# Kernel tuning notes

Measured on AMD Instinct MI355X. Metric: run time of the kernel, lower is better.

Reference implementation:

```python
import jax, jax.numpy as jnp
import numpy as np

IN_FEATURES = 4096
OUT_FEATURES = 16384
BATCH, SEQ = 2, 2048


def make_24_mask(w):
    # 2:4 structured mask: keep the 2 largest-magnitude entries of each
    # contiguous group of 4 along the in_features axis (like bdense2sparse).
    o, i = w.shape
    g = jnp.abs(w).reshape(o, i // 4, 4)
    # rank within each group; keep top-2
    idx = jnp.argsort(g, axis=-1)  # ascending
    ranks = jnp.argsort(idx, axis=-1)
    mask = ranks >= 2
    return mask.reshape(o, i)


def setup_inputs() -> dict:
    key = jax.random.key(0)
    k1, k2, k3 = jax.random.split(key, 3)
    x = jax.random.normal(k1, (BATCH, SEQ, IN_FEATURES), dtype=jnp.float32)
    weight = jax.random.normal(k2, (OUT_FEATURES, IN_FEATURES), dtype=jnp.float32) * (1.0 / np.sqrt(IN_FEATURES))
    mask = make_24_mask(weight)
    bias = jax.random.normal(k3, (OUT_FEATURES,), dtype=jnp.float32) * 0.01
    return {"x": x, "weight": weight, "mask": mask, "bias": bias}


def reference(x, weight, mask, bias):
    # 2:4 structured-sparse linear: y = x @ (mask * W).T + b
    w = weight * mask.astype(weight.dtype)
    out = jnp.einsum('bsi,oi->bso', x, w)  # [B, S, out_features]
    return out + bias
```

## Files before the change

kernel.cpp:

```cpp
#include <hip/hip_runtime.h>
#include <stdint.h>

#define M_DIM 4096
#define N_DIM 16384
#define K_DIM 4096

#define BM 128
#define BN 128
#define BK 64

typedef __attribute__((ext_vector_type(8))) short bf16x8;
typedef __attribute__((ext_vector_type(4))) float f32x4;


static __device__ __forceinline__ unsigned short f2bf(float f) {
    unsigned int u = __float_as_uint(f);
    return (unsigned short)((u + 0x7FFFu + ((u >> 16) & 1u)) >> 16);
}

typedef __attribute__((address_space(3))) void lds_void_t;
typedef const __attribute__((address_space(1))) void gbl_void_t;

static __device__ __forceinline__ void gload_lds16(const void* g, void* s) {
    __builtin_amdgcn_global_load_lds((gbl_void_t*)g, (lds_void_t*)s, 16, 0, 0);
}


__global__ void cvt_x_kernel(const float* __restrict__ x,
                             unsigned short* __restrict__ xb, int n8) {
    int i = blockIdx.x * blockDim.x + threadIdx.x;
    if (i >= n8) return;
    const float4 v0 = ((const float4*)x)[2 * i + 0];
    const float4 v1 = ((const float4*)x)[2 * i + 1];
    uint4 pk;
    pk.x = (unsigned)f2bf(v0.x) | ((unsigned)f2bf(v0.y) << 16);
    pk.y = (unsigned)f2bf(v0.z) | ((unsigned)f2bf(v0.w) << 16);
    pk.z = (unsigned)f2bf(v1.x) | ((unsigned)f2bf(v1.y) << 16);
    pk.w = (unsigned)f2bf(v1.z) | ((unsigned)f2bf(v1.w) << 16);
    ((uint4*)xb)[i] = pk;
}

__global__ void cvt_w_kernel(const float* __restrict__ w,
                             unsigned short* __restrict__ wb, int ngroups) {
    int g = blockIdx.x * blockDim.x + threadIdx.x;
    if (g >= ngroups) return;
    const float4 v = ((const float4*)w)[g];
    float a0 = fabsf(v.x), a1 = fabsf(v.y), a2 = fabsf(v.z), a3 = fabsf(v.w);
    int r0 = (a1 < a0) + (a2 < a0) + (a3 < a0);
    int r1 = (a0 < a1) + (a2 < a1) + (a3 < a1) + (a0 == a1);
    int r2 = (a0 < a2) + (a1 < a2) + (a3 < a2) + (a0 == a2) + (a1 == a2);
    int r3 = (a0 < a3) + (a1 < a3) + (a2 < a3) + (a0 == a3) + (a1 == a3) + (a2 == a3);
    unsigned short o0 = (r0 >= 2) ? f2bf(v.x) : (unsigned short)0;
    unsigned short o1 = (r1 >= 2) ? f2bf(v.y) : (unsigned short)0;
    unsigned short o2 = (r2 >= 2) ? f2bf(v.z) : (unsigned short)0;
    unsigned short o3 = (r3 >= 2) ? f2bf(v.w) : (unsigned short)0;
    uint2 pk;
    pk.x = (unsigned)o0 | ((unsigned)o1 << 16);
    pk.y = (unsigned)o2 | ((unsigned)o3 << 16);
    ((uint2*)wb)[g] = pk;
}


__global__ __launch_bounds__(256)
void gemm_bt_kernel(const unsigned short* __restrict__ A,
                    const unsigned short* __restrict__ B,
                    const float* __restrict__ bias,
                    float* __restrict__ C) {
    __shared__ unsigned short As[BM * BK];
    __shared__ unsigned short Bs[BN * BK];

    const int tid  = threadIdx.x;
    const int lane = tid & 63;
    const int wv   = tid >> 6;
    const int wm   = (wv >> 1) * 64;
    const int wn   = (wv & 1) * 64;

    const int nper = gridDim.x >> 3;
    int bid = blockIdx.x;
    int wg  = (bid & 7) * nper + (bid >> 3);
    const int tm = (wg >> 7) * BM;
    const int tn = (wg & 127) * BN;

    const int sub  = lane >> 3;
    const int clog = (lane & 7) ^ sub;

    const unsigned short* a_src[4];
    const unsigned short* b_src[4];
#pragma unroll
    for (int r = 0; r < 4; ++r) {
        int row = (wv * 4 + r) * 8 + sub;
        a_src[r] = A + (size_t)(tm + row) * K_DIM + clog * 8;
        b_src[r] = B + (size_t)(tn + row) * K_DIM + clog * 8;
    }

    const int frow = lane & 15;
    const int fk   = lane >> 4;

    f32x4 acc[4][4] = {};

    for (int k0 = 0; k0 < K_DIM; k0 += BK) {
#pragma unroll
        for (int r = 0; r < 4; ++r) {
            gload_lds16(a_src[r], &As[(wv * 4 + r) * 512]);
            gload_lds16(b_src[r], &Bs[(wv * 4 + r) * 512]);
            a_src[r] += BK;
            b_src[r] += BK;
        }
        __syncthreads();

#pragma unroll
        for (int kk = 0; kk < 2; ++kk) {
            bf16x8 af[4], bfr[4];
#pragma unroll
            for (int i = 0; i < 4; ++i) {
                int c = kk * 4 + fk;
                int ra = wm + i * 16 + frow;
                int pa = c ^ (ra & 7);
                af[i] = *(const bf16x8*)&As[ra * BK + pa * 8];
                int rb = wn + i * 16 + frow;
                int pb = c ^ (rb & 7);
                bfr[i] = *(const bf16x8*)&Bs[rb * BK + pb * 8];
            }
#pragma unroll
            for (int i = 0; i < 4; ++i)
#pragma unroll
                for (int j = 0; j < 4; ++j)
                    acc[i][j] = __builtin_amdgcn_mfma_f32_16x16x32_bf16(
                        af[i], bfr[j], acc[i][j], 0, 0, 0);
        }
        __syncthreads();
    }

    const int orow0 = tm + wm;
    const int ocol0 = tn + wn;
#pragma unroll
    for (int j = 0; j < 4; ++j) {
        int col = ocol0 + j * 16 + frow;
        float bj = bias[col];
#pragma unroll
        for (int i = 0; i < 4; ++i) {
            int rbase = orow0 + i * 16 + fk * 4;
            f32x4 v = acc[i][j];
#pragma unroll
            for (int r = 0; r < 4; ++r)
                C[(size_t)(rbase + r) * N_DIM + col] = v[r] + bj;
        }
    }
}

__global__ void naive_kernel(const float* __restrict__ x, const float* __restrict__ w,
                             const float* __restrict__ bias, float* __restrict__ out) {
    int n  = blockIdx.x;
    int m  = blockIdx.y * 256 + threadIdx.x;
    const float4* xr = (const float4*)(x + (size_t)m * K_DIM);
    const float4* wr = (const float4*)(w + (size_t)n * K_DIM);
    float s = 0.f;
    for (int g = 0; g < K_DIM / 4; ++g) {
        float4 wv = wr[g];
        float4 xv = xr[g];
        float a0 = fabsf(wv.x), a1 = fabsf(wv.y), a2 = fabsf(wv.z), a3 = fabsf(wv.w);
        int r0 = (a1 < a0) + (a2 < a0) + (a3 < a0);
        int r1 = (a0 < a1) + (a2 < a1) + (a3 < a1) + (a0 == a1);
        int r2 = (a0 < a2) + (a1 < a2) + (a3 < a2) + (a0 == a2) + (a1 == a2);
        int r3 = (a0 < a3) + (a1 < a3) + (a2 < a3) + (a0 == a3) + (a1 == a3) + (a2 == a3);
        if (r0 >= 2) s += xv.x * wv.x;
        if (r1 >= 2) s += xv.y * wv.y;
        if (r2 >= 2) s += xv.z * wv.z;
        if (r3 >= 2) s += xv.w * wv.w;
    }
    out[(size_t)m * N_DIM + n] = s + bias[n];
}

extern "C" void kernel_launch(void* const* d_in, const int* in_sizes, int n_in,
                              void* d_out, int out_size, void* d_ws, size_t ws_size,
                              hipStream_t stream) {
    const float* x    = (const float*)d_in[0];
    const float* w    = (const float*)d_in[1];
    const float* bias = (const float*)d_in[3];
    float* out        = (float*)d_out;

    const size_t x_elems = (size_t)M_DIM * K_DIM;
    const size_t w_elems = (size_t)N_DIM * K_DIM;
    const size_t need    = (x_elems + w_elems) * sizeof(unsigned short);

    if (ws_size >= need) {
        unsigned short* xb = (unsigned short*)d_ws;
        unsigned short* wb = xb + x_elems;

        int n8 = (int)(x_elems / 8);
        cvt_x_kernel<<<(n8 + 255) / 256, 256, 0, stream>>>(x, xb, n8);
        int ng = (int)(w_elems / 4);
        cvt_w_kernel<<<(ng + 255) / 256, 256, 0, stream>>>(w, wb, ng);

        dim3 grid((M_DIM / BM) * (N_DIM / BN));
        gemm_bt_kernel<<<grid, 256, 0, stream>>>(xb, wb, bias, out);
    } else {
        dim3 grid(N_DIM, M_DIM / 256);
        naive_kernel<<<grid, 256, 0, stream>>>(x, w, bias, out);
    }
}
```

Baseline: 1.218 ms.

## Move to 256x256 eight-wave GEMM with double-buffered LDS and interleaved staging

Tiles grow from 128x128 to 256x256 per block with 512 threads (8 waves, each owning a 128x64 sub-tile). The LDS buffer is doubled, and global-to-LDS loads for tile t+2 are split across four MFMA phases, separated by barriers and s_setprio. The goal is to overlap memory traffic with matrix math and to raise arithmetic intensity per byte loaded. The trade-off is 128KB of LDS per block, which limits how many blocks fit per CU, plus higher register pressure from the 8x4 accumulator array and hand-tuned waitcnt/barrier ordering that is fragile. The block-to-tile mapping is also changed to group N tiles per XCD.

```diff
diff --git a/kernel.cpp b/kernel.cpp
--- a/kernel.cpp
+++ b/kernel.cpp
@@ -5,9 +5,10 @@
 #define N_DIM 16384
 #define K_DIM 4096
 
-#define BM 128
-#define BN 128
+#define BM 256
+#define BN 256
 #define BK 64
+#define NT (K_DIM / BK)
 
 typedef __attribute__((ext_vector_type(8))) short bf16x8;
 typedef __attribute__((ext_vector_type(4))) float f32x4;
@@ -24,6 +25,13 @@
 static __device__ __forceinline__ void gload_lds16(const void* g, void* s) {
     __builtin_amdgcn_global_load_lds((gbl_void_t*)g, (lds_void_t*)s, 16, 0, 0);
 }
+
+static __device__ __forceinline__ f32x4 mfma16(bf16x8 a, bf16x8 b, f32x4 c) {
+    return __builtin_amdgcn_mfma_f32_16x16x32_bf16(a, b, c, 0, 0, 0);
+}
+
+#define BAR   __builtin_amdgcn_s_barrier()
+#define LGKM0 asm volatile("s_waitcnt lgkmcnt(0)" ::: "memory")
 
 
 __global__ void cvt_x_kernel(const float* __restrict__ x,
@@ -61,75 +69,153 @@
 }
 
 
-__global__ __launch_bounds__(256)
+__global__ __launch_bounds__(512, 2)
 void gemm_bt_kernel(const unsigned short* __restrict__ A,
                     const unsigned short* __restrict__ B,
                     const float* __restrict__ bias,
                     float* __restrict__ C) {
-    __shared__ unsigned short As[BM * BK];
-    __shared__ unsigned short Bs[BN * BK];
+    __shared__ unsigned short As[2][BM][BK];
+    __shared__ unsigned short Bs[2][BN][BK];
 
     const int tid  = threadIdx.x;
     const int lane = tid & 63;
-    const int wv   = tid >> 6;
-    const int wm   = (wv >> 1) * 64;
-    const int wn   = (wv & 1) * 64;
-
-    const int nper = gridDim.x >> 3;
-    int bid = blockIdx.x;
-    int wg  = (bid & 7) * nper + (bid >> 3);
-    const int tm = (wg >> 7) * BM;
-    const int tn = (wg & 127) * BN;
+    const int wid  = tid >> 6;
+    const int wm   = (wid >> 2) * 128;
+    const int wn   = (wid & 3) * 64;
+
+    const int xcd  = blockIdx.x & 7;
+    const int loc  = blockIdx.x >> 3;
+    const int tm   = (loc >> 3) * BM;
+    const int tn   = (xcd * 8 + (loc & 7)) * BN;
 
     const int sub  = lane >> 3;
     const int clog = (lane & 7) ^ sub;
 
-    const unsigned short* a_src[4];
-    const unsigned short* b_src[4];
-#pragma unroll
-    for (int r = 0; r < 4; ++r) {
-        int row = (wv * 4 + r) * 8 + sub;
-        a_src[r] = A + (size_t)(tm + row) * K_DIM + clog * 8;
-        b_src[r] = B + (size_t)(tn + row) * K_DIM + clog * 8;
+    const unsigned short* pA[4];
+    const unsigned short* pB[4];
+#pragma unroll
+    for (int q = 0; q < 4; ++q) {
+        pA[q] = A + (size_t)(tm + q * 64 + wid * 8 + sub) * K_DIM + clog * 8;
+        pB[q] = B + (size_t)(tn + q * 64 + wid * 8 + sub) * K_DIM + clog * 8;
     }
 
     const int frow = lane & 15;
     const int fk   = lane >> 4;
-
-    f32x4 acc[4][4] = {};
-
-    for (int k0 = 0; k0 < K_DIM; k0 += BK) {
-#pragma unroll
-        for (int r = 0; r < 4; ++r) {
-            gload_lds16(a_src[r], &As[(wv * 4 + r) * 512]);
-            gload_lds16(b_src[r], &Bs[(wv * 4 + r) * 512]);
-            a_src[r] += BK;
-            b_src[r] += BK;
-        }
-        __syncthreads();
-
-#pragma unroll
-        for (int kk = 0; kk < 2; ++kk) {
-            bf16x8 af[4], bfr[4];
-#pragma unroll
-            for (int i = 0; i < 4; ++i) {
-                int c = kk * 4 + fk;
-                int ra = wm + i * 16 + frow;
-                int pa = c ^ (ra & 7);
-                af[i] = *(const bf16x8*)&As[ra * BK + pa * 8];
-                int rb = wn + i * 16 + frow;
-                int pb = c ^ (rb & 7);
-                bfr[i] = *(const bf16x8*)&Bs[rb * BK + pb * 8];
-            }
-#pragma unroll
-            for (int i = 0; i < 4; ++i)
-#pragma unroll
-                for (int j = 0; j < 4; ++j)
-                    acc[i][j] = __builtin_amdgcn_mfma_f32_16x16x32_bf16(
-                        af[i], bfr[j], acc[i][j], 0, 0, 0);
-        }
-        __syncthreads();
-    }
+    const int pc0  = (0 + fk) ^ (frow & 7);
+    const int pc1  = (4 + fk) ^ (frow & 7);
+
+    f32x4 acc[8][4] = {};
+
+#pragma unroll
+    for (int q = 0; q < 4; ++q) {
+        gload_lds16(pA[q], &As[0][q * 64 + wid * 8][0]);
+        gload_lds16(pB[q], &Bs[0][q * 64 + wid * 8][0]);
+    }
+#pragma unroll
+    for (int q = 0; q < 4; ++q) {
+        gload_lds16(pA[q] + BK, &As[1][q * 64 + wid * 8][0]);
+        gload_lds16(pB[q] + BK, &Bs[1][q * 64 + wid * 8][0]);
+    }
+    asm volatile("s_waitcnt vmcnt(8)" ::: "memory");
+    BAR;
+
+#define TILE_STEP(BUFC)                                                         \
+  {                                                                             \
+    const int  tt      = t + (BUFC);                                            \
+    const bool dostage = (tt + 2 < NT);                                         \
+    const int  koff    = (tt + 2) * BK;                                         \
+    bf16x8 alo[4][2], ahi[4][2], blo[2][2], bhi[2][2];                          \
+                          \
+    _Pragma("unroll")                                                           \
+    for (int i = 0; i < 4; ++i) {                                               \
+      alo[i][0] = *(const bf16x8*)&As[BUFC][wm + i * 16 + frow][pc0 * 8];       \
+      alo[i][1] = *(const bf16x8*)&As[BUFC][wm + i * 16 + frow][pc1 * 8];       \
+    }                                                                           \
+    _Pragma("unroll")                                                           \
+    for (int j = 0; j < 2; ++j) {                                               \
+      blo[j][0] = *(const bf16x8*)&Bs[BUFC][wn + j * 16 + frow][pc0 * 8];       \
+      blo[j][1] = *(const bf16x8*)&Bs[BUFC][wn + j * 16 + frow][pc1 * 8];       \
+    }                                                                           \
+    BAR; LGKM0;                                                                 \
+    __builtin_amdgcn_s_setprio(1);                                              \
+    _Pragma("unroll")                                                           \
+    for (int i = 0; i < 4; ++i)                                                 \
+      _Pragma("unroll")                                                         \
+      for (int j = 0; j < 2; ++j) {                                             \
+        acc[i][j] = mfma16(alo[i][0], blo[j][0], acc[i][j]);                    \
+        acc[i][j] = mfma16(alo[i][1], blo[j][1], acc[i][j]);                    \
+      }                                                                         \
+    __builtin_amdgcn_s_setprio(0);                                              \
+    BAR;                                                                        \
+    \
+    _Pragma("unroll")                                                           \
+    for (int i = 0; i < 4; ++i) {                                               \
+      ahi[i][0] = *(const bf16x8*)&As[BUFC][wm + 64 + i * 16 + frow][pc0 * 8];  \
+      ahi[i][1] = *(const bf16x8*)&As[BUFC][wm + 64 + i * 16 + frow][pc1 * 8];  \
+    }                                                                           \
+    _Pragma("unroll")                                                           \
+    for (int j = 0; j < 2; ++j) {                                               \
+      bhi[j][0] = *(const bf16x8*)&Bs[BUFC][wn + 32 + j * 16 + frow][pc0 * 8];  \
+      bhi[j][1] = *(const bf16x8*)&Bs[BUFC][wn + 32 + j * 16 + frow][pc1 * 8];  \
+    }                                                                           \
+    if (dostage) {                                                              \
+      gload_lds16(pA[0] + koff, &As[BUFC][0 * 64 + wid * 8][0]);                \
+      gload_lds16(pA[2] + koff, &As[BUFC][2 * 64 + wid * 8][0]);                \
+    }                                                                           \
+    BAR; LGKM0;                                                                 \
+    __builtin_amdgcn_s_setprio(1);                                              \
+    _Pragma("unroll")                                                           \
+    for (int i = 0; i < 4; ++i)                                                 \
+      _Pragma("unroll")                                                         \
+      for (int j = 0; j < 2; ++j) {                                             \
+        acc[i][2 + j] = mfma16(alo[i][0], bhi[j][0], acc[i][2 + j]);            \
+        acc[i][2 + j] = mfma16(alo[i][1], bhi[j][1], acc[i][2 + j]);            \
+      }                                                                         \
+    __builtin_amdgcn_s_setprio(0);                                              \
+    BAR;                                                                        \
+                     \
+    if (dostage) {                                                              \
+      gload_lds16(pA[1] + koff, &As[BUFC][1 * 64 + wid * 8][0]);                \
+      gload_lds16(pA[3] + koff, &As[BUFC][3 * 64 + wid * 8][0]);                \
+      gload_lds16(pB[0] + koff, &Bs[BUFC][0 * 64 + wid * 8][0]);                \
+    }                                                                           \
+    BAR; LGKM0;                                                                 \
+    __builtin_amdgcn_s_setprio(1);                                              \
+    _Pragma("unroll")                                                           \
+    for (int i = 0; i < 4; ++i)                                                 \
+      _Pragma("unroll")                                                         \
+      for (int j = 0; j < 2; ++j) {                                             \
+        acc[4 + i][j] = mfma16(ahi[i][0], blo[j][0], acc[4 + i][j]);            \
+        acc[4 + i][j] = mfma16(ahi[i][1], blo[j][1], acc[4 + i][j]);            \
+      }                                                                         \
+    __builtin_amdgcn_s_setprio(0);                                              \
+    BAR;                                                                        \
+              \
+    if (dostage) {                                                              \
+      gload_lds16(pB[1] + koff, &Bs[BUFC][1 * 64 + wid * 8][0]);                \
+      gload_lds16(pB[2] + koff, &Bs[BUFC][2 * 64 + wid * 8][0]);                \
+      gload_lds16(pB[3] + koff, &Bs[BUFC][3 * 64 + wid * 8][0]);                \
+    }                                                                           \
+    BAR; LGKM0;                                                                 \
+    __builtin_amdgcn_s_setprio(1);                                              \
+    _Pragma("unroll")                                                           \
+    for (int i = 0; i < 4; ++i)                                                 \
+      _Pragma("unroll")                                                         \
+      for (int j = 0; j < 2; ++j) {                                             \
+        acc[4 + i][2 + j] = mfma16(ahi[i][0], bhi[j][0], acc[4 + i][2 + j]);    \
+        acc[4 + i][2 + j] = mfma16(ahi[i][1], bhi[j][1], acc[4 + i][2 + j]);    \
+      }                                                                         \
+    __builtin_amdgcn_s_setprio(0);                                              \
+    if (dostage) { asm volatile("s_waitcnt vmcnt(8)" ::: "memory"); }           \
+    else         { asm volatile("s_waitcnt vmcnt(0)" ::: "memory"); }           \
+    BAR;                                                                        \
+  }
+
+    for (int t = 0; t < NT; t += 2) {
+        TILE_STEP(0)
+        TILE_STEP(1)
+    }
+#undef TILE_STEP
 
     const int orow0 = tm + wm;
     const int ocol0 = tn + wn;
@@ -138,9 +224,9 @@
         int col = ocol0 + j * 16 + frow;
         float bj = bias[col];
 #pragma unroll
-        for (int i = 0; i < 4; ++i) {
+        for (int i = 0; i < 8; ++i) {
+            f32x4 v = acc[i][j];
             int rbase = orow0 + i * 16 + fk * 4;
-            f32x4 v = acc[i][j];
 #pragma unroll
             for (int r = 0; r < 4; ++r)
                 C[(size_t)(rbase + r) * N_DIM + col] = v[r] + bj;
@@ -193,7 +279,7 @@
         cvt_w_kernel<<<(ng + 255) / 256, 256, 0, stream>>>(w, wb, ng);
 
         dim3 grid((M_DIM / BM) * (N_DIM / BN));
-        gemm_bt_kernel<<<grid, 256, 0, stream>>>(xb, wb, bias, out);
+        gemm_bt_kernel<<<grid, 512, 0, stream>>>(xb, wb, bias, out);
     } else {
         dim3 grid(N_DIM, M_DIM / 256);
         naive_kernel<<<grid, 256, 0, stream>>>(x, w, bias, out);
```

After: 1.300 ms. 6.7% more time.
